# Optimization experiments

Hardware: AMD Instinct MI355X
Metric: run time of the kernel (lower is better)

## Reference

```python
import jax, jax.numpy as jnp
import numpy as np

EMBED_DIM = 512
NUM_HEADS = 8
EDGE_THRESHOLD = 0.1


def setup_inputs() -> dict:
    key = jax.random.key(0)
    ks = jax.random.split(key, 8)
    E, H = EMBED_DIM, NUM_HEADS
    B, S = 2, 2048
    s = 0.02
    return {
        'hidden_states': jax.random.normal(ks[0], (B, S, E), jnp.float32),
        'Wq': jax.random.normal(ks[1], (E, E), jnp.float32) * s,
        'bq': jnp.zeros((E,), jnp.float32),
        'Wk': jax.random.normal(ks[2], (E, E), jnp.float32) * s,
        'bk': jnp.zeros((E,), jnp.float32),
        'Wv': jax.random.normal(ks[3], (E, E), jnp.float32) * s,
        'bv': jnp.zeros((E,), jnp.float32),
        'Wm1': jax.random.normal(ks[4], (E, E + H), jnp.float32) * s,
        'bm1': jnp.zeros((E,), jnp.float32),
        'Wm2': jax.random.normal(ks[5], (E, E), jnp.float32) * s,
        'bm2': jnp.zeros((E,), jnp.float32),
        'Wo': jax.random.normal(ks[6], (E, E), jnp.float32) * s,
        'bo': jnp.zeros((E,), jnp.float32),
    }


def reference(hidden_states, Wq, bq, Wk, bk, Wv, bv, Wm1, bm1, Wm2, bm2, Wo, bo):
    B, S, E = hidden_states.shape
    H = NUM_HEADS
    hd = E // H
    scale = 1.0 / np.sqrt(hd).astype(np.float32)
    x = hidden_states

    q = (x @ Wq.T + bq).reshape(B, S, H, hd)
    k = (x @ Wk.T + bk).reshape(B, S, H, hd)
    v = (x @ Wv.T + bv)  # kept flat [B,S,E]

    # edge weights: softmax over source nodes j, per head
    scores = jnp.einsum('bihd,bjhd->bijh', q, k) * scale  # [B,S,S,H]
    edge_weights = jax.nn.softmax(scores, axis=2)
    ew_mean = edge_weights.mean(axis=-1)  # [B,S,S]
    adjacency = (ew_mean > EDGE_THRESHOLD).astype(x.dtype)

    # message passing: mean of (edge-weighted features) over adjacent neighbors
    masked_w = ew_mean * adjacency
    aggregated = jnp.einsum('bij,bjd->bid', masked_w, x)
    num_neighbors = jnp.clip(adjacency.sum(axis=-1, keepdims=True), 1.0, None)
    messages = aggregated / num_neighbors

    # gated MLP over [node_features ; mean edge features]
    edge_features = edge_weights.mean(axis=2)  # [B,S,H]
    combined = jnp.concatenate([x, edge_features], axis=-1)
    h = jax.nn.gelu(combined @ Wm1.T + bm1, approximate=False)
    updated = (h @ Wm2.T + bm2) + messages

    attended = jnp.einsum('bij,bjd->bid', ew_mean, v)
    out = (updated + attended) @ Wo.T + bo  # dropout p=0 -> identity
    return out
```

## Files before the change

kernel.cpp:

```cpp
#include <hip/hip_runtime.h>
#include <hip/hip_bf16.h>
#include <math.h>

#define BB 2
#define SS 2048
#define EE 512
#define HH 8
#define NN (BB*SS)
#define JC1 8
#define JCP 4

typedef __attribute__((ext_vector_type(8))) short short8;
typedef __attribute__((ext_vector_type(4))) float f32x4;

__device__ __forceinline__ float b2f(short v){
    return __uint_as_float(((unsigned)(unsigned short)v) << 16);
}
__device__ __forceinline__ unsigned f2bf(float f){
    unsigned u = __float_as_uint(f);
    u += 0x7fffu + ((u >> 16) & 1u);
    return u >> 16;
}
__device__ __forceinline__ void stage16_f32(const float* __restrict__ src,
                                            __hip_bfloat16* dst){
    const float4 f0 = *reinterpret_cast<const float4*>(src);
    const float4 f1 = *reinterpret_cast<const float4*>(src + 4);
    const float4 f2 = *reinterpret_cast<const float4*>(src + 8);
    const float4 f3 = *reinterpret_cast<const float4*>(src + 12);
    uint4 o0, o1;
    o0.x = f2bf(f0.x) | (f2bf(f0.y) << 16);
    o0.y = f2bf(f0.z) | (f2bf(f0.w) << 16);
    o0.z = f2bf(f1.x) | (f2bf(f1.y) << 16);
    o0.w = f2bf(f1.z) | (f2bf(f1.w) << 16);
    o1.x = f2bf(f2.x) | (f2bf(f2.y) << 16);
    o1.y = f2bf(f2.z) | (f2bf(f2.w) << 16);
    o1.z = f2bf(f3.x) | (f2bf(f3.y) << 16);
    o1.w = f2bf(f3.z) | (f2bf(f3.w) << 16);
    *reinterpret_cast<uint4*>(dst) = o0;
    *reinterpret_cast<uint4*>(dst + 8) = o1;
}
__device__ __forceinline__ void stage16_b16(const __hip_bfloat16* __restrict__ src,
                                            __hip_bfloat16* dst){
    const uint4* s = reinterpret_cast<const uint4*>(src);
    uint4* d = reinterpret_cast<uint4*>(dst);
    d[0] = s[0]; d[1] = s[1];
}

__global__ void conv_bf16(
    const float* s0, const float* s1, const float* s2, const float* s3,
    const float* s4, const float* s5, const float* s6,
    __hip_bfloat16* d0, __hip_bfloat16* d1, __hip_bfloat16* d2, __hip_bfloat16* d3,
    __hip_bfloat16* d4, __hip_bfloat16* d5, __hip_bfloat16* d6)
{
    const int which = blockIdx.y;
    const float* s; __hip_bfloat16* d; int n;
    switch (which) {
        case 0: s = s0; d = d0; n = 2097152; break;
        case 1: s = s1; d = d1; n = 262144; break;
        case 2: s = s2; d = d2; n = 262144; break;
        case 3: s = s3; d = d3; n = 262144; break;
        case 4: s = s4; d = d4; n = 266240; break;
        case 5: s = s5; d = d5; n = 262144; break;
        default: s = s6; d = d6; n = 262144; break;
    }
    const int base = (blockIdx.x * 256 + threadIdx.x) * 4;
    if (base >= n) return;
    const float4 f = *reinterpret_cast<const float4*>(s + base);
    uint2 o;
    o.x = f2bf(f.x) | (f2bf(f.y) << 16);
    o.y = f2bf(f.z) | (f2bf(f.w) << 16);
    *reinterpret_cast<uint2*>(d + base) = o;
}

template<int B16>
__global__ __launch_bounds__(256) void qkv_gemm(
    const void* __restrict__ x,
    const void* __restrict__ Wq, const float* __restrict__ bq,
    const void* __restrict__ Wk, const float* __restrict__ bk,
    const void* __restrict__ Wv, const float* __restrict__ bv,
    __hip_bfloat16* __restrict__ qb,
    __hip_bfloat16* __restrict__ kb,
    __hip_bfloat16* __restrict__ vT)
{
    __shared__ __hip_bfloat16 As[64][72];
    __shared__ __hip_bfloat16 Bs[64][72];
    const int tid = threadIdx.x;
    const int which = blockIdx.x >> 3;
    const int col0 = (blockIdx.x & 7) * 64;
    const int row0 = blockIdx.y * 64;
    const int wv = tid >> 6, lane = tid & 63, quad = lane >> 4, m16 = lane & 15;
    const int sr = tid >> 2;
    const int sc = (tid & 3) * 16;
    const void* W    = (which == 0) ? Wq : (which == 1) ? Wk : Wv;
    const float* bias = (which == 0) ? bq : (which == 1) ? bk : bv;

    f32x4 acc[4];
    #pragma unroll
    for (int nt = 0; nt < 4; ++nt) acc[nt] = (f32x4){0.f, 0.f, 0.f, 0.f};

    for (int k0 = 0; k0 < 512; k0 += 64) {
        if (B16) {
            stage16_b16((const __hip_bfloat16*)x + (size_t)(row0 + sr) * EE + k0 + sc, &As[sr][sc]);
            stage16_b16((const __hip_bfloat16*)W + (size_t)(col0 + sr) * EE + k0 + sc, &Bs[sr][sc]);
        } else {
            stage16_f32((const float*)x + (size_t)(row0 + sr) * EE + k0 + sc, &As[sr][sc]);
            stage16_f32((const float*)W + (size_t)(col0 + sr) * EE + k0 + sc, &Bs[sr][sc]);
        }
        __syncthreads();
        #pragma unroll
        for (int ks = 0; ks < 2; ++ks) {
            const short8 a = *reinterpret_cast<const short8*>(
                &As[wv * 16 + m16][ks * 32 + quad * 8]);
            #pragma unroll
            for (int nt = 0; nt < 4; ++nt) {
                const short8 b = *reinterpret_cast<const short8*>(
                    &Bs[nt * 16 + m16][ks * 32 + quad * 8]);
                acc[nt] = __builtin_amdgcn_mfma_f32_16x16x32_bf16(a, b, acc[nt], 0, 0, 0);
            }
        }
        __syncthreads();
    }

    if (which == 2) {
        #pragma unroll
        for (int nt = 0; nt < 4; ++nt) {
            const float bb = bias[col0 + nt * 16 + m16];
            #pragma unroll
            for (int r = 0; r < 4; ++r)
                Bs[wv * 16 + quad * 4 + r][nt * 16 + m16] =
                    __float2bfloat16(acc[nt][r] + bb);
        }
        __syncthreads();
        const int bb2 = row0 >> 11;
        const int j0 = row0 & (SS - 1);
        const int er = tid >> 2;
        const int js = (tid & 3) * 16;
        unsigned pk[8];
        #pragma unroll
        for (int p = 0; p < 8; ++p) {
            const unsigned lo = *reinterpret_cast<const unsigned short*>(&Bs[js + 2*p][er]);
            const unsigned hi = *reinterpret_cast<const unsigned short*>(&Bs[js + 2*p + 1][er]);
            pk[p] = lo | (hi << 16);
        }
        uint4 s0; s0.x = pk[0]; s0.y = pk[1]; s0.z = pk[2]; s0.w = pk[3];
        uint4 s1; s1.x = pk[4]; s1.y = pk[5]; s1.z = pk[6]; s1.w = pk[7];
        __hip_bfloat16* dst = vT + ((size_t)(bb2 * EE + col0 + er)) * SS + j0 + js;
        *reinterpret_cast<uint4*>(dst) = s0;
        *reinterpret_cast<uint4*>(dst + 8) = s1;
    } else {
        __hip_bfloat16* C = (which == 0) ? qb : kb;
        #pragma unroll
        for (int nt = 0; nt < 4; ++nt) {
            const int gn = col0 + nt * 16 + m16;
            const float bb = bias[gn];
            #pragma unroll
            for (int r = 0; r < 4; ++r) {
                const int gm = row0 + wv * 16 + quad * 4 + r;
                C[(size_t)gm * EE + gn] = __float2bfloat16(acc[nt][r] + bb);
            }
        }
    }
}

template<int MODE, int AB16, int WB16, int CF32>
__global__ __launch_bounds__(256) void gemm_bt(
    const void* __restrict__ Av,
    const void* __restrict__ Wv_,
    const float* __restrict__ bias,
    void* __restrict__ Cv,
    int ldb)
{
    __shared__ __hip_bfloat16 As[64][72];
    __shared__ __hip_bfloat16 Bs[64][72];
    const int tid = threadIdx.x;
    const int col0 = blockIdx.x * 64;
    const int row0 = blockIdx.y * 64;
    const int wv = tid >> 6, lane = tid & 63, quad = lane >> 4, m16 = lane & 15;
    const int sr = tid >> 2;
    const int sc = (tid & 3) * 16;

    f32x4 acc[4];
    #pragma unroll
    for (int nt = 0; nt < 4; ++nt) acc[nt] = (f32x4){0.f, 0.f, 0.f, 0.f};

    for (int k0 = 0; k0 < 512; k0 += 64) {
        if (AB16)
            stage16_b16((const __hip_bfloat16*)Av + (size_t)(row0 + sr) * EE + k0 + sc, &As[sr][sc]);
        else
            stage16_f32((const float*)Av + (size_t)(row0 + sr) * EE + k0 + sc, &As[sr][sc]);
        if (WB16)
            stage16_b16((const __hip_bfloat16*)Wv_ + (size_t)(col0 + sr) * ldb + k0 + sc, &Bs[sr][sc]);
        else
            stage16_f32((const float*)Wv_ + (size_t)(col0 + sr) * ldb + k0 + sc, &Bs[sr][sc]);
        __syncthreads();
        #pragma unroll
        for (int ks = 0; ks < 2; ++ks) {
            const short8 a = *reinterpret_cast<const short8*>(
                &As[wv * 16 + m16][ks * 32 + quad * 8]);
            #pragma unroll
            for (int nt = 0; nt < 4; ++nt) {
                const short8 b = *reinterpret_cast<const short8*>(
                    &Bs[nt * 16 + m16][ks * 32 + quad * 8]);
                acc[nt] = __builtin_amdgcn_mfma_f32_16x16x32_bf16(a, b, acc[nt], 0, 0, 0);
            }
        }
        __syncthreads();
    }

    #pragma unroll
    for (int nt = 0; nt < 4; ++nt) {
        const int gn = col0 + nt * 16 + m16;
        float bb = bias[gn];
        if (MODE == 1) {
            float ts = 0.f;
            #pragma unroll
            for (int h = 0; h < 8; ++h) {
                const size_t wi = (size_t)gn * ldb + 512 + h;
                ts += WB16 ? (float)((const __hip_bfloat16*)Wv_)[wi]
                           : ((const float*)Wv_)[wi];
            }
            bb += ts * (1.0f / (float)SS);
        }
        #pragma unroll
        for (int r = 0; r < 4; ++r) {
            const int gm = row0 + wv * 16 + quad * 4 + r;
            const size_t ci = (size_t)gm * EE + gn;
            float c = acc[nt][r] + bb;
            if (MODE == 1) c = 0.5f * c * (1.0f + erff(c * 0.70710678118654752f));
            if (MODE == 2) c += (float)((const __hip_bfloat16*)Cv)[ci];
            if (CF32) ((float*)Cv)[ci] = c;
            else      ((__hip_bfloat16*)Cv)[ci] = __float2bfloat16(c);
        }
    }
}

__global__ __launch_bounds__(256) void attn_denoms(
    const __hip_bfloat16* __restrict__ qws,
    const __hip_bfloat16* __restrict__ kws,
    float* __restrict__ dnP,
    int* __restrict__ cntI)
{
    __shared__ __hip_bfloat16 KL[2][16][520];
    const int tid = threadIdx.x;
    const int wv = tid >> 6, lane = tid & 63, quad = lane >> 4, m16 = lane & 15;
    const int jc = blockIdx.x;
    const int it = blockIdx.y;
    const int b  = blockIdx.z;
    const size_t g0 = (size_t)b * SS + it * 64;
    const size_t gb = (size_t)b * SS;

    if (jc == 0 && tid < 64) cntI[g0 + tid] = 0;

    short8 aq[HH][2];
    #pragma unroll
    for (int h = 0; h < HH; ++h)
        #pragma unroll
        for (int ks = 0; ks < 2; ++ks)
            aq[h][ks] = *reinterpret_cast<const short8*>(
                qws + (g0 + wv * 16 + m16) * EE + h * 64 + ks * 32 + quad * 8);

    float dph[HH][4];
    #pragma unroll
    for (int h = 0; h < HH; ++h)
        #pragma unroll
        for (int r = 0; r < 4; ++r) dph[h][r] = 0.f;

    const int srow = tid >> 4, scol = (tid & 15) * 32;
    {
        const uint4* src = reinterpret_cast<const uint4*>(
            kws + (gb + jc * 256 + srow) * EE + scol);
        uint4* dst = reinterpret_cast<uint4*>(&KL[0][srow][scol]);
        dst[0] = src[0]; dst[1] = src[1]; dst[2] = src[2]; dst[3] = src[3];
    }

    for (int jt = 0; jt < 16; ++jt) {
        __syncthreads();
        uint4 kr[4];
        if (jt + 1 < 16) {
            const uint4* src = reinterpret_cast<const uint4*>(
                kws + (gb + jc * 256 + (jt + 1) * 16 + srow) * EE + scol);
            kr[0] = src[0]; kr[1] = src[1]; kr[2] = src[2]; kr[3] = src[3];
        }
        #pragma unroll
        for (int h = 0; h < HH; ++h) {
            const short8 b0 = *reinterpret_cast<const short8*>(&KL[jt & 1][m16][h * 64 + quad * 8]);
            const short8 b1 = *reinterpret_cast<const short8*>(&KL[jt & 1][m16][h * 64 + 32 + quad * 8]);
            f32x4 c = {0.f, 0.f, 0.f, 0.f};
            c = __builtin_amdgcn_mfma_f32_16x16x32_bf16(aq[h][0], b0, c, 0, 0, 0);
            c = __builtin_amdgcn_mfma_f32_16x16x32_bf16(aq[h][1], b1, c, 0, 0, 0);
            #pragma unroll
            for (int r = 0; r < 4; ++r) dph[h][r] += __expf(c[r] * 0.125f);
        }
        if (jt + 1 < 16) {
            uint4* dst = reinterpret_cast<uint4*>(&KL[(jt + 1) & 1][srow][scol]);
            dst[0] = kr[0]; dst[1] = kr[1]; dst[2] = kr[2]; dst[3] = kr[3];
        }
    }

    #pragma unroll
    for (int h = 0; h < HH; ++h)
        #pragma unroll
        for (int off = 1; off <= 8; off <<= 1)
            #pragma unroll
            for (int r = 0; r < 4; ++r) dph[h][r] += __shfl_xor(dph[h][r], off, 64);
    if (m16 == 0) {
        const size_t i = (size_t)it * 64 + wv * 16 + quad * 4;
        #pragma unroll
        for (int h = 0; h < HH; ++h)
            #pragma unroll
            for (int r = 0; r < 4; ++r)
                dnP[((size_t)(jc * BB + b) * SS + i + r) * HH + h] = dph[h][r];
    }
}

__global__ __launch_bounds__(256, 2) void attn_ewpv(
    const __hip_bfloat16* __restrict__ qws,
    const __hip_bfloat16* __restrict__ kws,
    const __hip_bfloat16* __restrict__ vTg,
    const float* __restrict__ dnP,
    int* __restrict__ cntI,
    int* __restrict__ slotJ,
    float* __restrict__ slotW,
    __hip_bfloat16* __restrict__ pvP)
{
    __shared__ __hip_bfloat16 KL[32][520];
    __shared__ __hip_bfloat16 ewT[32][40];
    __shared__ float invd[HH][32];
    const int tid = threadIdx.x;
    const int wv = tid >> 6, lane = tid & 63, quad = lane >> 4, m16 = lane & 15;
    const int jc = blockIdx.x;
    const int it = blockIdx.y;
    const int b  = blockIdx.z;
    const size_t gb = (size_t)b * SS;
    const size_t g0 = gb + it * 32;
    const int ih = wv & 1;
    const int jh = wv >> 1;

    {
        const int h = tid >> 5, i = tid & 31;
        float s = 0.f;
        #pragma unroll
        for (int c = 0; c < JC1; ++c)
            s += dnP[((size_t)(c * BB + b) * SS + it * 32 + i) * HH + h];
        invd[h][i] = 0.125f / s;
    }

    short8 aq[HH][2];
    #pragma unroll
    for (int h = 0; h < HH; ++h)
        #pragma unroll
        for (int ks = 0; ks < 2; ++ks)
            aq[h][ks] = *reinterpret_cast<const short8*>(
                qws + (g0 + ih * 16 + m16) * EE + h * 64 + ks * 32 + quad * 8);

    f32x4 acc[2][8];
    #pragma unroll
    for (int mf = 0; mf < 2; ++mf)
        #pragma unroll
        for (int nf = 0; nf < 8; ++nf) acc[mf][nf] = (f32x4){0.f, 0.f, 0.f, 0.f};

    const int krow = tid >> 4, kcol = (tid & 15) * 32;
    const __hip_bfloat16* vrow0 = vTg + ((size_t)b * EE + wv * 128 + m16) * SS + quad * 8;

    for (int st = 0; st < 16; ++st) {
        const int j0 = jc * 512 + st * 32;
        #pragma unroll
        for (int rr = 0; rr < 2; ++rr) {
            const uint4* src = reinterpret_cast<const uint4*>(
                kws + (gb + j0 + rr * 16 + krow) * EE + kcol);
            uint4* dst = reinterpret_cast<uint4*>(&KL[rr * 16 + krow][kcol]);
            dst[0] = src[0]; dst[1] = src[1]; dst[2] = src[2]; dst[3] = src[3];
        }
        __syncthreads();

        float wsum[4] = {0.f, 0.f, 0.f, 0.f};
        #pragma unroll
        for (int h = 0; h < HH; ++h) {
            const short8 b0 = *reinterpret_cast<const short8*>(
                &KL[jh * 16 + m16][h * 64 + quad * 8]);
            const short8 b1 = *reinterpret_cast<const short8*>(
                &KL[jh * 16 + m16][h * 64 + 32 + quad * 8]);
            f32x4 c = {0.f, 0.f, 0.f, 0.f};
            c = __builtin_amdgcn_mfma_f32_16x16x32_bf16(aq[h][0], b0, c, 0, 0, 0);
            c = __builtin_amdgcn_mfma_f32_16x16x32_bf16(aq[h][1], b1, c, 0, 0, 0);
            #pragma unroll
            for (int r = 0; r < 4; ++r)
                wsum[r] += __expf(c[r] * 0.125f) * invd[h][ih * 16 + quad * 4 + r];
        }
        #pragma unroll
        for (int r = 0; r < 4; ++r) {
            const __hip_bfloat16 wb = __float2bfloat16(wsum[r]);
            ewT[ih * 16 + quad * 4 + r][jh * 16 + m16] = wb;
            if ((float)wb > 0.1f) {
                const int li = ih * 16 + quad * 4 + r;
                const int idx = atomicAdd(&cntI[g0 + li], 1);
                if (idx < 16) {
                    slotJ[((size_t)g0 + li) * 16 + idx] = j0 + jh * 16 + m16;
                    slotW[((size_t)g0 + li) * 16 + idx] = (float)wb;
                }
            }
        }
        __syncthreads();

        {
            short8 vb[8];
            #pragma unroll
            for (int nf = 0; nf < 8; ++nf)
                vb[nf] = *reinterpret_cast<const short8*>(vrow0 + (size_t)(nf * 16) * SS + j0);
            const short8 a0 = *reinterpret_cast<const short8*>(&ewT[m16][quad * 8]);
            const short8 a1 = *reinterpret_cast<const short8*>(&ewT[16 + m16][quad * 8]);
            #pragma unroll
            for (int nf = 0; nf < 8; ++nf) {
                acc[0][nf] = __builtin_amdgcn_mfma_f32_16x16x32_bf16(a0, vb[nf], acc[0][nf], 0, 0, 0);
                acc[1][nf] = __builtin_amdgcn_mfma_f32_16x16x32_bf16(a1, vb[nf], acc[1][nf], 0, 0, 0);
            }
        }
    }

    #pragma unroll
    for (int mf = 0; mf < 2; ++mf)
        #pragma unroll
        for (int nf = 0; nf < 8; ++nf)
            #pragma unroll
            for (int r = 0; r < 4; ++r)
                KL[mf * 16 + quad * 4 + r][wv * 128 + nf * 16 + m16] =
                    __float2bfloat16(acc[mf][nf][r]);
    __syncthreads();
    const int orow = tid >> 3;
    const int oc = (tid & 7) * 64;
    const uint4* s = reinterpret_cast<const uint4*>(&KL[orow][oc]);
    uint4* d = reinterpret_cast<uint4*>(
        pvP + ((size_t)jc * NN + g0 + orow) * EE + oc);
    #pragma unroll
    for (int q = 0; q < 8; ++q) d[q] = s[q];
}

__global__ __launch_bounds__(256) void pv_combine(
    const __hip_bfloat16* __restrict__ pvP,
    const int* __restrict__ cntI,
    const int* __restrict__ slotJ,
    const float* __restrict__ slotW,
    const float* __restrict__ x,
    __hip_bfloat16* __restrict__ u1out)
{
    const int tid = threadIdx.x;
    const int row = blockIdx.x * 4 + (tid >> 6);
    const int e0 = (tid & 63) * 8;
    float s[8] = {0.f, 0.f, 0.f, 0.f, 0.f, 0.f, 0.f, 0.f};
    #pragma unroll
    for (int c = 0; c < JCP; ++c) {
        const short8 v = *reinterpret_cast<const short8*>(
            pvP + ((size_t)c * NN + row) * EE + e0);
        #pragma unroll
        for (int k = 0; k < 8; ++k) s[k] += b2f(v[k]);
    }
    const int cn = cntI[row];
    if (cn > 0) {
        const float inv = 1.f / (float)cn;
        const int ns = cn < 16 ? cn : 16;
        const int b = row >> 11;
        for (int t = 0; t < ns; ++t) {
            const int j = slotJ[(size_t)row * 16 + t];
            const float w = slotW[(size_t)row * 16 + t] * inv;
            const float* xr = x + ((size_t)b * SS + j) * EE + e0;
            #pragma unroll
            for (int k = 0; k < 8; ++k) s[k] += w * xr[k];
        }
    }
    short8 o;
    #pragma unroll
    for (int k = 0; k < 8; ++k) o[k] = (short)f2bf(s[k]);
    *reinterpret_cast<short8*>(u1out + (size_t)row * EE + e0) = o;
}

extern "C" void kernel_launch(void* const* d_in, const int* in_sizes, int n_in,
                              void* d_out, int out_size, void* d_ws, size_t ws_size,
                              hipStream_t stream)
{
    const float* x   = (const float*)d_in[0];
    const float* Wq  = (const float*)d_in[1];
    const float* bq  = (const float*)d_in[2];
    const float* Wk  = (const float*)d_in[3];
    const float* bk  = (const float*)d_in[4];
    const float* Wv  = (const float*)d_in[5];
    const float* bv  = (const float*)d_in[6];
    const float* Wm1 = (const float*)d_in[7];
    const float* bm1 = (const float*)d_in[8];
    const float* Wm2 = (const float*)d_in[9];
    const float* bm2 = (const float*)d_in[10];
    const float* Wo  = (const float*)d_in[11];
    const float* bo  = (const float*)d_in[12];

    char* ws = (char*)d_ws;
    const size_t MB = 1024 * 1024;
    __hip_bfloat16* qb = (__hip_bfloat16*)(ws + 0);
    __hip_bfloat16* kb = (__hip_bfloat16*)(ws + 4*MB);
    __hip_bfloat16* vT = (__hip_bfloat16*)(ws + 8*MB);
    __hip_bfloat16* pvP = (__hip_bfloat16*)(ws + 12*MB);
    float* dnP = (float*)(ws + 28*MB);
    int*   cntI = (int*)(ws + 29*MB);
    int*   slotJ = (int*)(ws + 29*MB + 64*1024);
    float* slotW = (float*)(ws + 29*MB + 384*1024);
    const bool EXT = (ws_size >= 38 * MB);
    __hip_bfloat16* xb   = (__hip_bfloat16*)(ws + 30*MB);
    __hip_bfloat16* wqb  = (__hip_bfloat16*)(ws + 34*MB);
    __hip_bfloat16* wkb  = (__hip_bfloat16*)(ws + 34*MB + 512*1024);
    __hip_bfloat16* wvb  = (__hip_bfloat16*)(ws + 35*MB);
    __hip_bfloat16* wm1b = (__hip_bfloat16*)(ws + 35*MB + 512*1024);
    __hip_bfloat16* wm2b = (__hip_bfloat16*)(ws + 36*MB + 256*1024);
    __hip_bfloat16* wob  = (__hip_bfloat16*)(ws + 36*MB + 768*1024);

    dim3 blk(256, 1, 1);
    dim3 gg(EE / 64, NN / 64, 1);

    if (EXT) {
        conv_bf16<<<dim3(2048, 7, 1), blk, 0, stream>>>(
            x, Wq, Wk, Wv, Wm1, Wm2, Wo, xb, wqb, wkb, wvb, wm1b, wm2b, wob);
        qkv_gemm<1><<<dim3(24, NN / 64, 1), blk, 0, stream>>>(
            xb, wqb, bq, wkb, bk, wvb, bv, qb, kb, vT);
    } else {
        qkv_gemm<0><<<dim3(24, NN / 64, 1), blk, 0, stream>>>(
            x, Wq, bq, Wk, bk, Wv, bv, qb, kb, vT);
    }
    attn_denoms<<<dim3(JC1, SS / 64, BB), blk, 0, stream>>>(qb, kb, dnP, cntI);
    attn_ewpv<<<dim3(JCP, SS / 32, BB), blk, 0, stream>>>(
        qb, kb, vT, dnP, cntI, slotJ, slotW, pvP);
    pv_combine<<<dim3(NN / 4, 1, 1), blk, 0, stream>>>(
        pvP, cntI, slotJ, slotW, x, qb);
    if (EXT) {
        gemm_bt<1,1,1,0><<<gg, blk, 0, stream>>>(xb, wm1b, bm1, kb, EE + HH);
        gemm_bt<2,1,1,0><<<gg, blk, 0, stream>>>(kb, wm2b, bm2, qb, EE);
        gemm_bt<0,1,1,1><<<gg, blk, 0, stream>>>(qb, wob, bo, d_out, EE);
    } else {
        gemm_bt<1,0,0,0><<<gg, blk, 0, stream>>>(x, Wm1, bm1, kb, EE + HH);
        gemm_bt<2,1,0,0><<<gg, blk, 0, stream>>>(kb, Wm2, bm2, qb, EE);
        gemm_bt<0,1,0,1><<<gg, blk, 0, stream>>>(qb, Wo, bo, d_out, EE);
    }
}
```

Measured before the change: 231.7 us.

## Widen attn_ewpv to 512 threads with 64-key steps and coalesced K staging

attn_ewpv now runs 8 waves per block and processes 64 source keys per step instead of 32. Each wave covers a 64-wide slice of V columns, using two MFMA k-steps per accumulator, which halves the loop trip count and the number of barriers per key. K-tile staging in both attention kernels switches from per-thread contiguous 64-byte chunks to interleaved 16-byte chunks, aiming for better global coalescing and fewer LDS bank conflicts. The cost is more LDS per block (a 64-row K tile and a wider ewT) and a launch bound of 512 threads with min 4 blocks, which may limit registers per thread.

```diff
diff --git a/kernel.cpp b/kernel.cpp
--- a/kernel.cpp
+++ b/kernel.cpp
@@ -265,21 +265,23 @@
         #pragma unroll
         for (int r = 0; r < 4; ++r) dph[h][r] = 0.f;
 
-    const int srow = tid >> 4, scol = (tid & 15) * 32;
+    const int srow = tid >> 4, t4 = tid & 15;
     {
-        const uint4* src = reinterpret_cast<const uint4*>(
-            kws + (gb + jc * 256 + srow) * EE + scol);
-        uint4* dst = reinterpret_cast<uint4*>(&KL[0][srow][scol]);
-        dst[0] = src[0]; dst[1] = src[1]; dst[2] = src[2]; dst[3] = src[3];
+        #pragma unroll
+        for (int k = 0; k < 4; ++k)
+            *reinterpret_cast<uint4*>(&KL[0][srow][t4 * 8 + k * 128]) =
+                *reinterpret_cast<const uint4*>(
+                    kws + (gb + jc * 256 + srow) * EE + t4 * 8 + k * 128);
     }
 
     for (int jt = 0; jt < 16; ++jt) {
         __syncthreads();
         uint4 kr[4];
         if (jt + 1 < 16) {
-            const uint4* src = reinterpret_cast<const uint4*>(
-                kws + (gb + jc * 256 + (jt + 1) * 16 + srow) * EE + scol);
-            kr[0] = src[0]; kr[1] = src[1]; kr[2] = src[2]; kr[3] = src[3];
+            #pragma unroll
+            for (int k = 0; k < 4; ++k)
+                kr[k] = *reinterpret_cast<const uint4*>(
+                    kws + (gb + jc * 256 + (jt + 1) * 16 + srow) * EE + t4 * 8 + k * 128);
         }
         #pragma unroll
         for (int h = 0; h < HH; ++h) {
@@ -292,8 +294,9 @@
             for (int r = 0; r < 4; ++r) dph[h][r] += __expf(c[r] * 0.125f);
         }
         if (jt + 1 < 16) {
-            uint4* dst = reinterpret_cast<uint4*>(&KL[(jt + 1) & 1][srow][scol]);
-            dst[0] = kr[0]; dst[1] = kr[1]; dst[2] = kr[2]; dst[3] = kr[3];
+            #pragma unroll
+            for (int k = 0; k < 4; ++k)
+                *reinterpret_cast<uint4*>(&KL[(jt + 1) & 1][srow][t4 * 8 + k * 128]) = kr[k];
         }
     }
 
@@ -313,7 +316,7 @@
     }
 }
 
-__global__ __launch_bounds__(256, 2) void attn_ewpv(
+__global__ __launch_bounds__(512, 4) void attn_ewpv(
     const __hip_bfloat16* __restrict__ qws,
     const __hip_bfloat16* __restrict__ kws,
     const __hip_bfloat16* __restrict__ vTg,
@@ -323,8 +326,8 @@
     float* __restrict__ slotW,
     __hip_bfloat16* __restrict__ pvP)
 {
-    __shared__ __hip_bfloat16 KL[32][520];
-    __shared__ __hip_bfloat16 ewT[32][40];
+    __shared__ __hip_bfloat16 KL[64][520];
+    __shared__ __hip_bfloat16 ewT[32][72];
     __shared__ float invd[HH][32];
     const int tid = threadIdx.x;
     const int wv = tid >> 6, lane = tid & 63, quad = lane >> 4, m16 = lane & 15;
@@ -334,9 +337,9 @@
     const size_t gb = (size_t)b * SS;
     const size_t g0 = gb + it * 32;
     const int ih = wv & 1;
-    const int jh = wv >> 1;
-
-    {
+    const int jq = wv >> 1;
+
+    if (tid < HH * 32) {
         const int h = tid >> 5, i = tid & 31;
         float s = 0.f;
         #pragma unroll
@@ -353,33 +356,31 @@
             aq[h][ks] = *reinterpret_cast<const short8*>(
                 qws + (g0 + ih * 16 + m16) * EE + h * 64 + ks * 32 + quad * 8);
 
-    f32x4 acc[2][8];
+    f32x4 acc[2][4];
     #pragma unroll
     for (int mf = 0; mf < 2; ++mf)
         #pragma unroll
-        for (int nf = 0; nf < 8; ++nf) acc[mf][nf] = (f32x4){0.f, 0.f, 0.f, 0.f};
-
-    const int krow = tid >> 4, kcol = (tid & 15) * 32;
-    const __hip_bfloat16* vrow0 = vTg + ((size_t)b * EE + wv * 128 + m16) * SS + quad * 8;
-
-    for (int st = 0; st < 16; ++st) {
-        const int j0 = jc * 512 + st * 32;
-        #pragma unroll
-        for (int rr = 0; rr < 2; ++rr) {
-            const uint4* src = reinterpret_cast<const uint4*>(
-                kws + (gb + j0 + rr * 16 + krow) * EE + kcol);
-            uint4* dst = reinterpret_cast<uint4*>(&KL[rr * 16 + krow][kcol]);
-            dst[0] = src[0]; dst[1] = src[1]; dst[2] = src[2]; dst[3] = src[3];
-        }
+        for (int nf = 0; nf < 4; ++nf) acc[mf][nf] = (f32x4){0.f, 0.f, 0.f, 0.f};
+
+    const int srow8 = tid >> 3, t8 = tid & 7;
+    const __hip_bfloat16* vrow0 = vTg + ((size_t)b * EE + wv * 64 + m16) * SS + quad * 8;
+
+    for (int st = 0; st < 8; ++st) {
+        const int j0 = jc * 512 + st * 64;
+        #pragma unroll
+        for (int k = 0; k < 8; ++k)
+            *reinterpret_cast<uint4*>(&KL[srow8][t8 * 8 + k * 64]) =
+                *reinterpret_cast<const uint4*>(
+                    kws + (gb + j0 + srow8) * EE + t8 * 8 + k * 64);
         __syncthreads();
 
         float wsum[4] = {0.f, 0.f, 0.f, 0.f};
         #pragma unroll
         for (int h = 0; h < HH; ++h) {
             const short8 b0 = *reinterpret_cast<const short8*>(
-                &KL[jh * 16 + m16][h * 64 + quad * 8]);
+                &KL[jq * 16 + m16][h * 64 + quad * 8]);
             const short8 b1 = *reinterpret_cast<const short8*>(
-                &KL[jh * 16 + m16][h * 64 + 32 + quad * 8]);
+                &KL[jq * 16 + m16][h * 64 + 32 + quad * 8]);
             f32x4 c = {0.f, 0.f, 0.f, 0.f};
             c = __builtin_amdgcn_mfma_f32_16x16x32_bf16(aq[h][0], b0, c, 0, 0, 0);
             c = __builtin_amdgcn_mfma_f32_16x16x32_bf16(aq[h][1], b1, c, 0, 0, 0);
@@ -390,12 +391,12 @@
         #pragma unroll
         for (int r = 0; r < 4; ++r) {
             const __hip_bfloat16 wb = __float2bfloat16(wsum[r]);
-            ewT[ih * 16 + quad * 4 + r][jh * 16 + m16] = wb;
+            ewT[ih * 16 + quad * 4 + r][jq * 16 + m16] = wb;
             if ((float)wb > 0.1f) {
                 const int li = ih * 16 + quad * 4 + r;
                 const int idx = atomicAdd(&cntI[g0 + li], 1);
                 if (idx < 16) {
-                    slotJ[((size_t)g0 + li) * 16 + idx] = j0 + jh * 16 + m16;
+                    slotJ[((size_t)g0 + li) * 16 + idx] = j0 + jq * 16 + m16;
                     slotW[((size_t)g0 + li) * 16 + idx] = (float)wb;
                 }
             }
@@ -403,16 +404,19 @@
         __syncthreads();
 
         {
-            short8 vb[8];
-            #pragma unroll
-            for (int nf = 0; nf < 8; ++nf)
-                vb[nf] = *reinterpret_cast<const short8*>(vrow0 + (size_t)(nf * 16) * SS + j0);
-            const short8 a0 = *reinterpret_cast<const short8*>(&ewT[m16][quad * 8]);
-            const short8 a1 = *reinterpret_cast<const short8*>(&ewT[16 + m16][quad * 8]);
-            #pragma unroll
-            for (int nf = 0; nf < 8; ++nf) {
-                acc[0][nf] = __builtin_amdgcn_mfma_f32_16x16x32_bf16(a0, vb[nf], acc[0][nf], 0, 0, 0);
-                acc[1][nf] = __builtin_amdgcn_mfma_f32_16x16x32_bf16(a1, vb[nf], acc[1][nf], 0, 0, 0);
+            short8 a00 = *reinterpret_cast<const short8*>(&ewT[m16][quad * 8]);
+            short8 a01 = *reinterpret_cast<const short8*>(&ewT[m16][32 + quad * 8]);
+            short8 a10 = *reinterpret_cast<const short8*>(&ewT[16 + m16][quad * 8]);
+            short8 a11 = *reinterpret_cast<const short8*>(&ewT[16 + m16][32 + quad * 8]);
+            #pragma unroll
+            for (int nf = 0; nf < 4; ++nf) {
+                const __hip_bfloat16* vp = vrow0 + (size_t)(nf * 16) * SS + j0;
+                const short8 vb0 = *reinterpret_cast<const short8*>(vp);
+                const short8 vb1 = *reinterpret_cast<const short8*>(vp + 32);
+                acc[0][nf] = __builtin_amdgcn_mfma_f32_16x16x32_bf16(a00, vb0, acc[0][nf], 0, 0, 0);
+                acc[0][nf] = __builtin_amdgcn_mfma_f32_16x16x32_bf16(a01, vb1, acc[0][nf], 0, 0, 0);
+                acc[1][nf] = __builtin_amdgcn_mfma_f32_16x16x32_bf16(a10, vb0, acc[1][nf], 0, 0, 0);
+                acc[1][nf] = __builtin_amdgcn_mfma_f32_16x16x32_bf16(a11, vb1, acc[1][nf], 0, 0, 0);
             }
         }
     }
@@ -420,19 +424,19 @@
     #pragma unroll
     for (int mf = 0; mf < 2; ++mf)
         #pragma unroll
-        for (int nf = 0; nf < 8; ++nf)
+        for (int nf = 0; nf < 4; ++nf)
             #pragma unroll
             for (int r = 0; r < 4; ++r)
-                KL[mf * 16 + quad * 4 + r][wv * 128 + nf * 16 + m16] =
+                KL[mf * 16 + quad * 4 + r][wv * 64 + nf * 16 + m16] =
                     __float2bfloat16(acc[mf][nf][r]);
     __syncthreads();
-    const int orow = tid >> 3;
-    const int oc = (tid & 7) * 64;
+    const int orow = tid >> 4;
+    const int oc = (tid & 15) * 32;
     const uint4* s = reinterpret_cast<const uint4*>(&KL[orow][oc]);
     uint4* d = reinterpret_cast<uint4*>(
         pvP + ((size_t)jc * NN + g0 + orow) * EE + oc);
     #pragma unroll
-    for (int q = 0; q < 8; ++q) d[q] = s[q];
+    for (int q = 0; q < 4; ++q) d[q] = s[q];
 }
 
 __global__ __launch_bounds__(256) void pv_combine(
@@ -511,6 +515,7 @@
     __hip_bfloat16* wob  = (__hip_bfloat16*)(ws + 36*MB + 768*1024);
 
     dim3 blk(256, 1, 1);
+    dim3 blk512(512, 1, 1);
     dim3 gg(EE / 64, NN / 64, 1);
 
     if (EXT) {
@@ -523,7 +528,7 @@
             x, Wq, bq, Wk, bk, Wv, bv, qb, kb, vT);
     }
     attn_denoms<<<dim3(JC1, SS / 64, BB), blk, 0, stream>>>(qb, kb, dnP, cntI);
-    attn_ewpv<<<dim3(JCP, SS / 32, BB), blk, 0, stream>>>(
+    attn_ewpv<<<dim3(JCP, SS / 32, BB), blk512, 0, stream>>>(
         qb, kb, vT, dnP, cntI, slotJ, slotW, pvP);
     pv_combine<<<dim3(NN / 4, 1, 1), blk, 0, stream>>>(
         pvP, cntI, slotJ, slotW, x, qb);
```

New measurement: 286.0 us. +23.4%, slower.

## Use async global-to-LDS loads with XOR swizzle and double buffering in attention kernels

Applied to the files above, without the earlier changes.

Both attention kernels now stage K tiles with global_load_lds, which writes straight into LDS, into an XOR-swizzled unpadded layout. attn_ewpv gains double-buffered K and edge-weight tiles, so the next tile's load is issued while the current one is computed, and one barrier per step is removed. The aim is to hide global load latency, free registers used for staging, and avoid LDS bank conflicts. The larger LDS footprint in attn_ewpv and the dropped occupancy hint in launch_bounds may lower occupancy.

```diff
diff --git a/kernel.cpp b/kernel.cpp
--- a/kernel.cpp
+++ b/kernel.cpp
@@ -12,6 +12,8 @@
 
 typedef __attribute__((ext_vector_type(8))) short short8;
 typedef __attribute__((ext_vector_type(4))) float f32x4;
+typedef const __attribute__((address_space(1))) unsigned int gu32;
+typedef __attribute__((address_space(3))) unsigned int lu32;
 
 __device__ __forceinline__ float b2f(short v){
     return __uint_as_float(((unsigned)(unsigned short)v) << 16);
@@ -240,7 +242,7 @@
     float* __restrict__ dnP,
     int* __restrict__ cntI)
 {
-    __shared__ __hip_bfloat16 KL[2][16][520];
+    __shared__ __hip_bfloat16 KLs[2][16][512];
     const int tid = threadIdx.x;
     const int wv = tid >> 6, lane = tid & 63, quad = lane >> 4, m16 = lane & 15;
     const int jc = blockIdx.x;
@@ -265,36 +267,46 @@
         #pragma unroll
         for (int r = 0; r < 4; ++r) dph[h][r] = 0.f;
 
-    const int srow = tid >> 4, scol = (tid & 15) * 32;
     {
-        const uint4* src = reinterpret_cast<const uint4*>(
-            kws + (gb + jc * 256 + srow) * EE + scol);
-        uint4* dst = reinterpret_cast<uint4*>(&KL[0][srow][scol]);
-        dst[0] = src[0]; dst[1] = src[1]; dst[2] = src[2]; dst[3] = src[3];
-    }
+        #pragma unroll
+        for (int rr = 0; rr < 4; ++rr) {
+            const int row = wv * 4 + rr;
+            const __hip_bfloat16* g = kws + (gb + jc * 256 + row) * EE
+                                      + ((lane ^ (row & 7)) << 3);
+            __builtin_amdgcn_global_load_lds(
+                (gu32*)(const void*)g, (lu32*)(void*)&KLs[0][row][0], 16, 0, 0);
+        }
+    }
+    __syncthreads();
 
     for (int jt = 0; jt < 16; ++jt) {
-        __syncthreads();
-        uint4 kr[4];
         if (jt + 1 < 16) {
-            const uint4* src = reinterpret_cast<const uint4*>(
-                kws + (gb + jc * 256 + (jt + 1) * 16 + srow) * EE + scol);
-            kr[0] = src[0]; kr[1] = src[1]; kr[2] = src[2]; kr[3] = src[3];
-        }
+            #pragma unroll
+            for (int rr = 0; rr < 4; ++rr) {
+                const int row = wv * 4 + rr;
+                const __hip_bfloat16* g = kws + (gb + jc * 256 + (jt + 1) * 16 + row) * EE
+                                          + ((lane ^ (row & 7)) << 3);
+                __builtin_amdgcn_global_load_lds(
+                    (gu32*)(const void*)g,
+                    (lu32*)(void*)&KLs[(jt + 1) & 1][row][0], 16, 0, 0);
+            }
+        }
+        const int cur = jt & 1;
+        const char* kp = (const char*)&KLs[cur][m16][0];
+        const int sw = (m16 & 7) << 4;
         #pragma unroll
         for (int h = 0; h < HH; ++h) {
-            const short8 b0 = *reinterpret_cast<const short8*>(&KL[jt & 1][m16][h * 64 + quad * 8]);
-            const short8 b1 = *reinterpret_cast<const short8*>(&KL[jt & 1][m16][h * 64 + 32 + quad * 8]);
+            const short8 b0 = *reinterpret_cast<const short8*>(
+                kp + ((h * 128 + quad * 16) ^ sw));
+            const short8 b1 = *reinterpret_cast<const short8*>(
+                kp + ((h * 128 + 64 + quad * 16) ^ sw));
             f32x4 c = {0.f, 0.f, 0.f, 0.f};
             c = __builtin_amdgcn_mfma_f32_16x16x32_bf16(aq[h][0], b0, c, 0, 0, 0);
             c = __builtin_amdgcn_mfma_f32_16x16x32_bf16(aq[h][1], b1, c, 0, 0, 0);
             #pragma unroll
             for (int r = 0; r < 4; ++r) dph[h][r] += __expf(c[r] * 0.125f);
         }
-        if (jt + 1 < 16) {
-            uint4* dst = reinterpret_cast<uint4*>(&KL[(jt + 1) & 1][srow][scol]);
-            dst[0] = kr[0]; dst[1] = kr[1]; dst[2] = kr[2]; dst[3] = kr[3];
-        }
+        __syncthreads();
     }
 
     #pragma unroll
@@ -313,7 +325,7 @@
     }
 }
 
-__global__ __launch_bounds__(256, 2) void attn_ewpv(
+__global__ __launch_bounds__(256) void attn_ewpv(
     const __hip_bfloat16* __restrict__ qws,
     const __hip_bfloat16* __restrict__ kws,
     const __hip_bfloat16* __restrict__ vTg,
@@ -323,8 +335,8 @@
     float* __restrict__ slotW,
     __hip_bfloat16* __restrict__ pvP)
 {
-    __shared__ __hip_bfloat16 KL[32][520];
-    __shared__ __hip_bfloat16 ewT[32][40];
+    __shared__ __hip_bfloat16 KLs[2][32][512];
+    __shared__ __hip_bfloat16 ewTd[2][32][40];
     __shared__ float invd[HH][32];
     const int tid = threadIdx.x;
     const int wv = tid >> 6, lane = tid & 63, quad = lane >> 4, m16 = lane & 15;
@@ -359,38 +371,58 @@
         #pragma unroll
         for (int nf = 0; nf < 8; ++nf) acc[mf][nf] = (f32x4){0.f, 0.f, 0.f, 0.f};
 
-    const int krow = tid >> 4, kcol = (tid & 15) * 32;
     const __hip_bfloat16* vrow0 = vTg + ((size_t)b * EE + wv * 128 + m16) * SS + quad * 8;
+
+    {
+        #pragma unroll
+        for (int rr = 0; rr < 8; ++rr) {
+            const int row = wv * 8 + rr;
+            const __hip_bfloat16* g = kws + (gb + jc * 512 + row) * EE
+                                      + ((lane ^ (row & 7)) << 3);
+            __builtin_amdgcn_global_load_lds(
+                (gu32*)(const void*)g, (lu32*)(void*)&KLs[0][row][0], 16, 0, 0);
+        }
+    }
+    __syncthreads();
 
     for (int st = 0; st < 16; ++st) {
         const int j0 = jc * 512 + st * 32;
-        #pragma unroll
-        for (int rr = 0; rr < 2; ++rr) {
-            const uint4* src = reinterpret_cast<const uint4*>(
-                kws + (gb + j0 + rr * 16 + krow) * EE + kcol);
-            uint4* dst = reinterpret_cast<uint4*>(&KL[rr * 16 + krow][kcol]);
-            dst[0] = src[0]; dst[1] = src[1]; dst[2] = src[2]; dst[3] = src[3];
-        }
-        __syncthreads();
+        if (st + 1 < 16) {
+            #pragma unroll
+            for (int rr = 0; rr < 8; ++rr) {
+                const int row = wv * 8 + rr;
+                const __hip_bfloat16* g = kws + (gb + j0 + 32 + row) * EE
+                                          + ((lane ^ (row & 7)) << 3);
+                __builtin_amdgcn_global_load_lds(
+                    (gu32*)(const void*)g,
+                    (lu32*)(void*)&KLs[(st + 1) & 1][row][0], 16, 0, 0);
+            }
+        }
+        const int cur = st & 1;
 
         float wsum[4] = {0.f, 0.f, 0.f, 0.f};
-        #pragma unroll
-        for (int h = 0; h < HH; ++h) {
-            const short8 b0 = *reinterpret_cast<const short8*>(
-                &KL[jh * 16 + m16][h * 64 + quad * 8]);
-            const short8 b1 = *reinterpret_cast<const short8*>(
-                &KL[jh * 16 + m16][h * 64 + 32 + quad * 8]);
-            f32x4 c = {0.f, 0.f, 0.f, 0.f};
-            c = __builtin_amdgcn_mfma_f32_16x16x32_bf16(aq[h][0], b0, c, 0, 0, 0);
-            c = __builtin_amdgcn_mfma_f32_16x16x32_bf16(aq[h][1], b1, c, 0, 0, 0);
-            #pragma unroll
-            for (int r = 0; r < 4; ++r)
-                wsum[r] += __expf(c[r] * 0.125f) * invd[h][ih * 16 + quad * 4 + r];
+        {
+            const int krow = jh * 16 + m16;
+            const char* kp = (const char*)&KLs[cur][krow][0];
+            const int sw = (krow & 7) << 4;
+            #pragma unroll
+            for (int h = 0; h < HH; ++h) {
+                const short8 b0 = *reinterpret_cast<const short8*>(
+                    kp + ((h * 128 + quad * 16) ^ sw));
+                const short8 b1 = *reinterpret_cast<const short8*>(
+                    kp + ((h * 128 + 64 + quad * 16) ^ sw));
+                f32x4 c = {0.f, 0.f, 0.f, 0.f};
+                c = __builtin_amdgcn_mfma_f32_16x16x32_bf16(aq[h][0], b0, c, 0, 0, 0);
+                c = __builtin_amdgcn_mfma_f32_16x16x32_bf16(aq[h][1], b1, c, 0, 0, 0);
+                #pragma unroll
+                for (int r = 0; r < 4; ++r)
+                    wsum[r] += __expf(c[r] * 0.125f) * invd[h][ih * 16 + quad * 4 + r];
+            }
         }
         #pragma unroll
         for (int r = 0; r < 4; ++r) {
             const __hip_bfloat16 wb = __float2bfloat16(wsum[r]);
-            ewT[ih * 16 + quad * 4 + r][jh * 16 + m16] = wb;
+            ewTd[cur][ih * 16 + quad * 4 + r][jh * 16 + m16] = wb;
             if ((float)wb > 0.1f) {
                 const int li = ih * 16 + quad * 4 + r;
                 const int idx = atomicAdd(&cntI[g0 + li], 1);
@@ -407,8 +439,8 @@
             #pragma unroll
             for (int nf = 0; nf < 8; ++nf)
                 vb[nf] = *reinterpret_cast<const short8*>(vrow0 + (size_t)(nf * 16) * SS + j0);
-            const short8 a0 = *reinterpret_cast<const short8*>(&ewT[m16][quad * 8]);
-            const short8 a1 = *reinterpret_cast<const short8*>(&ewT[16 + m16][quad * 8]);
+            const short8 a0 = *reinterpret_cast<const short8*>(&ewTd[cur][m16][quad * 8]);
+            const short8 a1 = *reinterpret_cast<const short8*>(&ewTd[cur][16 + m16][quad * 8]);
             #pragma unroll
             for (int nf = 0; nf < 8; ++nf) {
                 acc[0][nf] = __builtin_amdgcn_mfma_f32_16x16x32_bf16(a0, vb[nf], acc[0][nf], 0, 0, 0);
@@ -422,17 +454,25 @@
         #pragma unroll
         for (int nf = 0; nf < 8; ++nf)
             #pragma unroll
-            for (int r = 0; r < 4; ++r)
-                KL[mf * 16 + quad * 4 + r][wv * 128 + nf * 16 + m16] =
+            for (int r = 0; r < 4; ++r) {
+                const int row = mf * 16 + quad * 4 + r;
+                const int cb = (wv * 128 + nf * 16 + m16) * 2;
+                *reinterpret_cast<__hip_bfloat16*>(
+                    (char*)&KLs[0][row][0] + (cb ^ ((row & 7) << 4))) =
                     __float2bfloat16(acc[mf][nf][r]);
+            }
     __syncthreads();
-    const int orow = tid >> 3;
-    const int oc = (tid & 7) * 64;
-    const uint4* s = reinterpret_cast<const uint4*>(&KL[orow][oc]);
-    uint4* d = reinterpret_cast<uint4*>(
-        pvP + ((size_t)jc * NN + g0 + orow) * EE + oc);
-    #pragma unroll
-    for (int q = 0; q < 8; ++q) d[q] = s[q];
+    {
+        const int orow = tid >> 3;
+        const int ocb = (tid & 7) * 128;
+        const int sw2 = (orow & 7) << 4;
+        uint4* d = reinterpret_cast<uint4*>(
+            pvP + ((size_t)jc * NN + g0 + orow) * EE + (tid & 7) * 64);
+        #pragma unroll
+        for (int q = 0; q < 8; ++q)
+            d[q] = *reinterpret_cast<const uint4*>(
+                (const char*)&KLs[0][orow][0] + ((ocb + q * 16) ^ sw2));
+    }
 }
 
 __global__ __launch_bounds__(256) void pv_combine(
```

After: 255.2 us. 10.1% more time.

## Split attn_ewpv output columns across two blocks and coalesce K tile loads

Applied to the files above, without the earlier changes.

The edge-weight/PV kernel now launches twice as many blocks, and each one computes half of the 512 value columns. The point is more parallelism and fewer accumulator registers per thread, which should help occupancy. The cost is that both halves recompute the QK scores and exp weights, and only the first half records adjacency slots. Separately, the K-tile staging in attn_denoms now uses interleaved 16-byte loads across threads, so global accesses coalesce better.

```diff
diff --git a/kernel.cpp b/kernel.cpp
--- a/kernel.cpp
+++ b/kernel.cpp
@@ -265,21 +265,23 @@
         #pragma unroll
         for (int r = 0; r < 4; ++r) dph[h][r] = 0.f;
 
-    const int srow = tid >> 4, scol = (tid & 15) * 32;
+    const int srow = tid >> 4, t4 = tid & 15;
     {
-        const uint4* src = reinterpret_cast<const uint4*>(
-            kws + (gb + jc * 256 + srow) * EE + scol);
-        uint4* dst = reinterpret_cast<uint4*>(&KL[0][srow][scol]);
-        dst[0] = src[0]; dst[1] = src[1]; dst[2] = src[2]; dst[3] = src[3];
+        #pragma unroll
+        for (int k = 0; k < 4; ++k)
+            *reinterpret_cast<uint4*>(&KL[0][srow][t4 * 8 + k * 128]) =
+                *reinterpret_cast<const uint4*>(
+                    kws + (gb + jc * 256 + srow) * EE + t4 * 8 + k * 128);
     }
 
     for (int jt = 0; jt < 16; ++jt) {
         __syncthreads();
         uint4 kr[4];
         if (jt + 1 < 16) {
-            const uint4* src = reinterpret_cast<const uint4*>(
-                kws + (gb + jc * 256 + (jt + 1) * 16 + srow) * EE + scol);
-            kr[0] = src[0]; kr[1] = src[1]; kr[2] = src[2]; kr[3] = src[3];
+            #pragma unroll
+            for (int k = 0; k < 4; ++k)
+                kr[k] = *reinterpret_cast<const uint4*>(
+                    kws + (gb + jc * 256 + (jt + 1) * 16 + srow) * EE + t4 * 8 + k * 128);
         }
         #pragma unroll
         for (int h = 0; h < HH; ++h) {
@@ -292,8 +294,9 @@
             for (int r = 0; r < 4; ++r) dph[h][r] += __expf(c[r] * 0.125f);
         }
         if (jt + 1 < 16) {
-            uint4* dst = reinterpret_cast<uint4*>(&KL[(jt + 1) & 1][srow][scol]);
-            dst[0] = kr[0]; dst[1] = kr[1]; dst[2] = kr[2]; dst[3] = kr[3];
+            #pragma unroll
+            for (int k = 0; k < 4; ++k)
+                *reinterpret_cast<uint4*>(&KL[(jt + 1) & 1][srow][t4 * 8 + k * 128]) = kr[k];
         }
     }
 
@@ -328,7 +331,9 @@
     __shared__ float invd[HH][32];
     const int tid = threadIdx.x;
     const int wv = tid >> 6, lane = tid & 63, quad = lane >> 4, m16 = lane & 15;
-    const int jc = blockIdx.x;
+    const int bx = blockIdx.x;
+    const int jc = bx >> 1;
+    const int eh = bx & 1;
     const int it = blockIdx.y;
     const int b  = blockIdx.z;
     const size_t gb = (size_t)b * SS;
@@ -353,14 +358,15 @@
             aq[h][ks] = *reinterpret_cast<const short8*>(
                 qws + (g0 + ih * 16 + m16) * EE + h * 64 + ks * 32 + quad * 8);
 
-    f32x4 acc[2][8];
+    f32x4 acc[2][4];
     #pragma unroll
     for (int mf = 0; mf < 2; ++mf)
         #pragma unroll
-        for (int nf = 0; nf < 8; ++nf) acc[mf][nf] = (f32x4){0.f, 0.f, 0.f, 0.f};
+        for (int nf = 0; nf < 4; ++nf) acc[mf][nf] = (f32x4){0.f, 0.f, 0.f, 0.f};
 
     const int krow = tid >> 4, kcol = (tid & 15) * 32;
-    const __hip_bfloat16* vrow0 = vTg + ((size_t)b * EE + wv * 128 + m16) * SS + quad * 8;
+    const __hip_bfloat16* vrow0 =
+        vTg + ((size_t)b * EE + eh * 256 + wv * 64 + m16) * SS + quad * 8;
 
     for (int st = 0; st < 16; ++st) {
         const int j0 = jc * 512 + st * 32;
@@ -391,7 +397,7 @@
         for (int r = 0; r < 4; ++r) {
             const __hip_bfloat16 wb = __float2bfloat16(wsum[r]);
             ewT[ih * 16 + quad * 4 + r][jh * 16 + m16] = wb;
-            if ((float)wb > 0.1f) {
+            if (eh == 0 && (float)wb > 0.1f) {
                 const int li = ih * 16 + quad * 4 + r;
                 const int idx = atomicAdd(&cntI[g0 + li], 1);
                 if (idx < 16) {
@@ -403,14 +409,14 @@
         __syncthreads();
 
         {
-            short8 vb[8];
-            #pragma unroll
-            for (int nf = 0; nf < 8; ++nf)
+            short8 vb[4];
+            #pragma unroll
+            for (int nf = 0; nf < 4; ++nf)
                 vb[nf] = *reinterpret_cast<const short8*>(vrow0 + (size_t)(nf * 16) * SS + j0);
             const short8 a0 = *reinterpret_cast<const short8*>(&ewT[m16][quad * 8]);
             const short8 a1 = *reinterpret_cast<const short8*>(&ewT[16 + m16][quad * 8]);
             #pragma unroll
-            for (int nf = 0; nf < 8; ++nf) {
+            for (int nf = 0; nf < 4; ++nf) {
                 acc[0][nf] = __builtin_amdgcn_mfma_f32_16x16x32_bf16(a0, vb[nf], acc[0][nf], 0, 0, 0);
                 acc[1][nf] = __builtin_amdgcn_mfma_f32_16x16x32_bf16(a1, vb[nf], acc[1][nf], 0, 0, 0);
             }
@@ -420,19 +426,20 @@
     #pragma unroll
     for (int mf = 0; mf < 2; ++mf)
         #pragma unroll
-        for (int nf = 0; nf < 8; ++nf)
+        for (int nf = 0; nf < 4; ++nf)
             #pragma unroll
             for (int r = 0; r < 4; ++r)
-                KL[mf * 16 + quad * 4 + r][wv * 128 + nf * 16 + m16] =
+                KL[mf * 16 + quad * 4 + r][wv * 64 + nf * 16 + m16] =
                     __float2bfloat16(acc[mf][nf][r]);
     __syncthreads();
     const int orow = tid >> 3;
-    const int oc = (tid & 7) * 64;
+    const int oc = (tid & 7) * 32;
     const uint4* s = reinterpret_cast<const uint4*>(&KL[orow][oc]);
     uint4* d = reinterpret_cast<uint4*>(
-        pvP + ((size_t)jc * NN + g0 + orow) * EE + oc);
-    #pragma unroll
-    for (int q = 0; q < 8; ++q) d[q] = s[q];
+        pvP + ((size_t)jc * NN + g0 + orow) * EE + eh * 256 + oc);
+    #pragma unroll
+    for (int q = 0; q < 4; ++q) d[q] = s[q];
+
 }
 
 __global__ __launch_bounds__(256) void pv_combine(
@@ -523,7 +530,7 @@
             x, Wq, bq, Wk, bk, Wv, bv, qb, kb, vT);
     }
     attn_denoms<<<dim3(JC1, SS / 64, BB), blk, 0, stream>>>(qb, kb, dnP, cntI);
-    attn_ewpv<<<dim3(JCP, SS / 32, BB), blk, 0, stream>>>(
+    attn_ewpv<<<dim3(JCP * 2, SS / 32, BB), blk, 0, stream>>>(
         qb, kb, vT, dnP, cntI, slotJ, slotW, pvP);
     pv_combine<<<dim3(NN / 4, 1, 1), blk, 0, stream>>>(
         pvP, cntI, slotJ, slotW, x, qb);
```

Result: slower. 261.1 us (+12.7%).
